# Kernel optimization log

Measured on AMD Instinct MI355X. Metric: run time of the kernel, lower is better.

## Reference

```python
import jax, jax.numpy as jnp
import numpy as np

B, S, D, H = 2, 2048, 1024, 16
HD = D // H  # head dim = 64


def setup_inputs() -> dict:
    key = jax.random.key(0)
    ks = jax.random.split(key, 9)
    sc = 1.0 / np.sqrt(D)
    x = jax.random.normal(ks[0], (B, S, D), dtype=jnp.float32)
    # weights stored as (in, out); y = x @ W + b (same math as torch Linear with W.T)
    Wq = jax.random.normal(ks[1], (D, D), dtype=jnp.float32) * sc
    Wk = jax.random.normal(ks[2], (D, D), dtype=jnp.float32) * sc
    Wv = jax.random.normal(ks[3], (D, D), dtype=jnp.float32) * sc
    Wo = jax.random.normal(ks[4], (D, D), dtype=jnp.float32) * sc
    bq = jax.random.normal(ks[5], (D,), dtype=jnp.float32) * 0.01
    bk = jax.random.normal(ks[6], (D,), dtype=jnp.float32) * 0.01
    bv = jax.random.normal(ks[7], (D,), dtype=jnp.float32) * 0.01
    bo = jax.random.normal(ks[8], (D,), dtype=jnp.float32) * 0.01
    return {"x": x, "Wq": Wq, "bq": bq, "Wk": Wk, "bk": bk,
            "Wv": Wv, "bv": bv, "Wo": Wo, "bo": bo}


def reference(x, Wq, bq, Wk, bk, Wv, bv, Wo, bo):
    b, s, d = x.shape
    q = (x @ Wq + bq).reshape(b, s, H, HD)
    k = (x @ Wk + bk).reshape(b, s, H, HD)
    v = (x @ Wv + bv).reshape(b, s, H, HD)
    # [b, h, s, s] scores, scaled by sqrt(head_dim)
    scores = jnp.einsum('bqhd,bkhd->bhqk', q, k) / np.sqrt(HD)
    causal = jnp.triu(jnp.ones((s, s), dtype=bool), k=1)  # True above diagonal
    scores = jnp.where(causal, -jnp.inf, scores)
    w = jax.nn.softmax(scores, axis=-1)  # dropout rate 0 -> identity
    ctx = jnp.einsum('bhqk,bkhd->bqhd', w, v).reshape(b, s, d)
    return ctx @ Wo + bo
```

## Files before the change

kernel.cpp:

```cpp
#include <hip/hip_runtime.h>
#include <math.h>

#define BB 2
#define SS 2048
#define DD 1024
#define HH 16
#define HDIM 64

typedef __bf16 bf16_t;
typedef __attribute__((ext_vector_type(8))) __bf16 bf16x8;
typedef __attribute__((ext_vector_type(4))) __bf16 bf16x4;
typedef __attribute__((ext_vector_type(4))) float f32x4;

__device__ inline bf16_t f2bf(float f) {
    unsigned int x; __builtin_memcpy(&x, &f, 4);
    unsigned int r = (x + 0x7FFFu + ((x >> 16) & 1u)) >> 16;
    unsigned short us = (unsigned short)r;
    bf16_t b; __builtin_memcpy(&b, &us, 2); return b;
}
__device__ inline unsigned int fbits(float f) {
    unsigned int x; __builtin_memcpy(&x, &f, 4); return x;
}
__device__ inline unsigned int pack_bf2(float a, float b) {
    return ((fbits(a) + 0x8000u) >> 16) | ((fbits(b) + 0x8000u) & 0xFFFF0000u);
}
__device__ inline void gload16(const void* g, void* lds_base) {
    __builtin_amdgcn_global_load_lds(
        (const __attribute__((address_space(1))) void*)g,
        (__attribute__((address_space(3))) void*)lds_base, 16, 0, 0);
}

__global__ __launch_bounds__(256)
void prep_kernel(const float* __restrict__ x, bf16_t* __restrict__ xb,
                 const float* __restrict__ W0, const float* __restrict__ W1,
                 const float* __restrict__ W2, const float* __restrict__ W3,
                 bf16x8* __restrict__ P0, bf16x8* __restrict__ P1,
                 bf16x8* __restrict__ P2, bf16x8* __restrict__ P3) {
    const int bid = blockIdx.x, tid = threadIdx.x;
    if (bid < 2048) {
        const int i = bid * 512 + tid;
        #pragma unroll
        for (int u = 0; u < 2; ++u) {
            const int j = i + u * 256;
            const float4 v = reinterpret_cast<const float4*>(x)[j];
            bf16x4 o;
            o.x = f2bf(v.x); o.y = f2bf(v.y); o.z = f2bf(v.z); o.w = f2bf(v.w);
            reinterpret_cast<bf16x4*>(xb)[j] = o;
        }
    } else {
        const int t = (bid - 2048) * 256 + tid;
        const int g = t >> 10, n = t & 1023;
        const float* Ws[4] = {W0, W1, W2, W3};
        bf16x8* Pp[4] = {P0, P1, P2, P3};
        #pragma unroll
        for (int m = 0; m < 4; ++m) {
            bf16x8 v;
            #pragma unroll
            for (int j = 0; j < 8; ++j) v[j] = f2bf(Ws[m][(size_t)(g * 8 + j) * DD + n]);
            Pp[m][(size_t)g * DD + n] = v;
        }
    }
}

__global__ __launch_bounds__(256)
void gemm_qkv(const bf16_t* __restrict__ A,
              const bf16x8* __restrict__ Wp0, const bf16x8* __restrict__ Wp1,
              const bf16x8* __restrict__ Wp2,
              const float* __restrict__ b0, const float* __restrict__ b1,
              const float* __restrict__ b2,
              bf16_t* __restrict__ C0, bf16_t* __restrict__ C1,
              bf16_t* __restrict__ Vt) {
    __shared__ bf16x8 smem_v[4096];
    char* const smem = (char*)smem_v;

    const int z = blockIdx.z;
    const bf16x8* Wp = (z == 0) ? Wp0 : (z == 1) ? Wp1 : Wp2;
    const float* bias = (z == 0) ? b0 : (z == 1) ? b1 : b2;

    const int tid = threadIdx.x;
    const int ln = tid & 63, wv = tid >> 6;
    const int quad = ln >> 4, l15 = ln & 15;
    const int wr = wv >> 1, wc = wv & 1;
    const int m0 = blockIdx.y * 128;
    const int n0 = blockIdx.x * 128;

    int arow[4], acl[4], bg[4], bn[4];
    #pragma unroll
    for (int u = 0; u < 4; ++u) {
        const int S = (wv * 4 + u) * 64 + ln;
        arow[u] = S >> 3; acl[u] = (S & 7) ^ (arow[u] & 7);
        bg[u] = S >> 7;   bn[u] = S & 127;
    }

    f32x4 acc[4][4];
    #pragma unroll
    for (int i = 0; i < 4; ++i)
        #pragma unroll
        for (int j = 0; j < 4; ++j) acc[i][j] = (f32x4){0.f, 0.f, 0.f, 0.f};

    auto stage = [&](int k0, int buf) {
        char* const base = smem + buf * 32768;
        const int kg0 = k0 >> 3;
        #pragma unroll
        for (int u = 0; u < 4; ++u) {
            gload16(&A[(size_t)(m0 + arow[u]) * DD + k0 + acl[u] * 8],
                    base + (size_t)(wv * 4 + u) * 1024);
            gload16(&Wp[(size_t)(kg0 + bg[u]) * DD + n0 + bn[u]],
                    base + 16384 + (size_t)(wv * 4 + u) * 1024);
        }
    };

    stage(0, 0);
    __syncthreads();
    int cur = 0;
    for (int t = 0; t < 16; ++t) {
        const bf16x8 (*As)[8]   = reinterpret_cast<const bf16x8(*)[8]>(smem + cur * 32768);
        const bf16x8 (*Bs)[128] = reinterpret_cast<const bf16x8(*)[128]>(smem + cur * 32768 + 16384);
        bf16x8 fa[2][4], fb[2][4];
        #pragma unroll
        for (int kk = 0; kk < 2; ++kk) {
            #pragma unroll
            for (int mi = 0; mi < 4; ++mi) {
                const int row = wr * 64 + mi * 16 + l15;
                fa[kk][mi] = As[row][(kk * 4 + quad) ^ (row & 7)];
            }
            #pragma unroll
            for (int ni = 0; ni < 4; ++ni)
                fb[kk][ni] = Bs[kk * 4 + quad][wc * 64 + ni * 16 + l15];
        }
        if (t < 15) stage((t + 1) * 64, cur ^ 1);
        #pragma unroll
        for (int kk = 0; kk < 2; ++kk)
            #pragma unroll
            for (int mi = 0; mi < 4; ++mi)
                #pragma unroll
                for (int ni = 0; ni < 4; ++ni)
                    acc[mi][ni] = __builtin_amdgcn_mfma_f32_16x16x32_bf16(
                        fa[kk][mi], fb[kk][ni], acc[mi][ni], 0, 0, 0);
        if (t < 15) { __syncthreads(); cur ^= 1; }
    }

    if (z < 2) {
        bf16_t* C = (z == 0) ? C0 : C1;
        #pragma unroll
        for (int ni = 0; ni < 4; ++ni) {
            const int col = n0 + wc * 64 + ni * 16 + l15;
            const float bv = bias[col];
            #pragma unroll
            for (int mi = 0; mi < 4; ++mi)
                #pragma unroll
                for (int r = 0; r < 4; ++r) {
                    const int row = m0 + wr * 64 + mi * 16 + quad * 4 + r;
                    C[(size_t)row * DD + col] = f2bf(acc[mi][ni][r] + bv);
                }
        }
    } else {
        unsigned short (*T)[136] = reinterpret_cast<unsigned short(*)[136]>(smem);
        __syncthreads();
        #pragma unroll
        for (int ni = 0; ni < 4; ++ni) {
            const int cl = wc * 64 + ni * 16 + l15;
            const float bv = bias[n0 + cl];
            #pragma unroll
            for (int mi = 0; mi < 4; ++mi) {
                const int rl = wr * 64 + mi * 16 + quad * 4;
                uint2 pk;
                pk.x = pack_bf2(acc[mi][ni][0] + bv, acc[mi][ni][1] + bv);
                pk.y = pack_bf2(acc[mi][ni][2] + bv, acc[mi][ni][3] + bv);
                *reinterpret_cast<uint2*>(&T[cl][rl]) = pk;
            }
        }
        __syncthreads();
        const int b = m0 >> 11, s0 = m0 & 2047, h0 = n0 >> 6;
        #pragma unroll
        for (int u = 0; u < 8; ++u) {
            const int c = u * 256 + tid;
            const int s8 = c & 15, nl = c >> 4;
            const bf16x8 v = *reinterpret_cast<const bf16x8*>(&T[nl][s8 * 8]);
            const int bh = b * 16 + h0 + (nl >> 6), d = nl & 63;
            *reinterpret_cast<bf16x8*>(
                &Vt[((size_t)bh * 64 + d) * SS + s0 + s8 * 8]) = v;
        }
    }
}

__global__ __launch_bounds__(256)
void gemm_out(const bf16_t* __restrict__ A, const bf16x8* __restrict__ Wp,
              const float* __restrict__ bias, float* __restrict__ C) {
    __shared__ bf16x8 As[2][128][8];
    __shared__ bf16x8 Bs[2][8][64];

    const int tid = threadIdx.x;
    const int ln = tid & 63, wv = tid >> 6;
    const int quad = ln >> 4, l15 = ln & 15;
    const int wr = wv >> 1, wc = wv & 1;
    const int m0 = blockIdx.y * 128;
    const int n0 = blockIdx.x * 64;

    int arow[4], acl[4], bkg[2], bn[2];
    #pragma unroll
    for (int u = 0; u < 4; ++u) {
        const int S = (wv * 4 + u) * 64 + ln;
        arow[u] = S >> 3; acl[u] = (S & 7) ^ (arow[u] & 7);
    }
    #pragma unroll
    for (int u = 0; u < 2; ++u) {
        const int S = (wv * 2 + u) * 64 + ln;
        bkg[u] = S >> 6; bn[u] = S & 63;
    }

    f32x4 acc[4][2];
    #pragma unroll
    for (int i = 0; i < 4; ++i)
        #pragma unroll
        for (int j = 0; j < 2; ++j) acc[i][j] = (f32x4){0.f, 0.f, 0.f, 0.f};

    auto stage = [&](int k0, int buf) {
        const int kg0 = k0 >> 3;
        #pragma unroll
        for (int u = 0; u < 4; ++u)
            gload16(&A[(size_t)(m0 + arow[u]) * DD + k0 + acl[u] * 8],
                    (char*)&As[buf][0][0] + (size_t)(wv * 4 + u) * 1024);
        #pragma unroll
        for (int u = 0; u < 2; ++u)
            gload16(&Wp[(size_t)(kg0 + bkg[u]) * DD + n0 + bn[u]],
                    (char*)&Bs[buf][0][0] + (size_t)(wv * 2 + u) * 1024);
    };

    stage(0, 0);
    __syncthreads();
    int cur = 0;
    for (int t = 0; t < 16; ++t) {
        bf16x8 fa[2][4], fb[2][2];
        #pragma unroll
        for (int kk = 0; kk < 2; ++kk) {
            #pragma unroll
            for (int mi = 0; mi < 4; ++mi) {
                const int row = wr * 64 + mi * 16 + l15;
                fa[kk][mi] = As[cur][row][(kk * 4 + quad) ^ (row & 7)];
            }
            #pragma unroll
            for (int ni = 0; ni < 2; ++ni)
                fb[kk][ni] = Bs[cur][kk * 4 + quad][wc * 32 + ni * 16 + l15];
        }
        if (t < 15) stage((t + 1) * 64, cur ^ 1);
        #pragma unroll
        for (int kk = 0; kk < 2; ++kk)
            #pragma unroll
            for (int mi = 0; mi < 4; ++mi)
                #pragma unroll
                for (int ni = 0; ni < 2; ++ni)
                    acc[mi][ni] = __builtin_amdgcn_mfma_f32_16x16x32_bf16(
                        fa[kk][mi], fb[kk][ni], acc[mi][ni], 0, 0, 0);
        if (t < 15) { __syncthreads(); cur ^= 1; }
    }

    #pragma unroll
    for (int ni = 0; ni < 2; ++ni) {
        const int col = n0 + wc * 32 + ni * 16 + l15;
        const float bv = bias[col];
        #pragma unroll
        for (int mi = 0; mi < 4; ++mi)
            #pragma unroll
            for (int r = 0; r < 4; ++r) {
                const int row = m0 + wr * 64 + mi * 16 + quad * 4 + r;
                C[(size_t)row * DD + col] = acc[mi][ni][r] + bv;
            }
    }
}

#define SCL 0.18033688f
#define FM  12.0f

__global__ __launch_bounds__(256)
void attn_mfma(const bf16_t* __restrict__ Q, const bf16_t* __restrict__ Kg,
               const bf16_t* __restrict__ Vt, bf16_t* __restrict__ Ctx) {
    __shared__ bf16x8 Ks[2][128][8];
    __shared__ bf16x8 Vs[2][128][8];
    __shared__ unsigned short Ps[4][2][16][64];

    const int tid = threadIdx.x;
    const int ln = tid & 63, w = tid >> 6;
    const int quad = ln >> 4, l15 = ln & 15;
    const int bh = blockIdx.x;
    const int tswz = (blockIdx.x + blockIdx.y) & 7;
    const int qt = (blockIdx.y < 8) ? tswz : 15 - tswz;
    const int b = bh >> 4, h = bh & 15;
    const size_t rowbase = (size_t)b * SS;
    const int col0 = h * 64;

    const int krow0 = w * 16 + (ln >> 3);
    const int krow1 = krow0 + 8;
    const int kc0 = (ln & 7) ^ (krow0 & 7);
    const int kc1 = (ln & 7) ^ (krow1 & 7);

    bf16x8 fq[2][2];
    #pragma unroll
    for (int rg = 0; rg < 2; ++rg) {
        const int qrow = qt * 128 + w * 32 + rg * 16 + l15;
        #pragma unroll
        for (int kk = 0; kk < 2; ++kk)
            fq[rg][kk] = *reinterpret_cast<const bf16x8*>(
                &Q[(rowbase + qrow) * DD + col0 + kk * 32 + quad * 8]);
    }

    f32x4 acc_o[2][4];
    #pragma unroll
    for (int rg = 0; rg < 2; ++rg)
        #pragma unroll
        for (int i = 0; i < 4; ++i) acc_o[rg][i] = (f32x4){0.f, 0.f, 0.f, 0.f};
    float lsum[2] = {0.f, 0.f};

    auto stage = [&](int tile, int half, int buf) {
        char* kb = (char*)&Ks[buf][half * 64][0] + w * 2048;
        char* vb = (char*)&Vs[buf][half * 64][0] + w * 2048;
        gload16(&Kg[(rowbase + tile * 64 + krow0) * DD + col0 + kc0 * 8], kb);
        gload16(&Kg[(rowbase + tile * 64 + krow1) * DD + col0 + kc1 * 8], kb + 1024);
        gload16(&Vt[((size_t)bh * 64 + krow0) * SS + tile * 64 + kc0 * 8], vb);
        gload16(&Vt[((size_t)bh * 64 + krow1) * SS + tile * 64 + kc1 * 8], vb + 1024);
    };

    const int swz = l15 & 7;

    auto compute_tile = [&](int buf, int ro, int dq0, int dq1) {
        const int dq[2] = {dq0, dq1};
        #pragma unroll
        for (int rg = 0; rg < 2; ++rg) {
            if (dq[rg] < 0) continue;
            unsigned short* const psw = &Ps[w][rg][l15][0];
            #pragma unroll
            for (int ni = 0; ni < 4; ++ni) {
                const int slot = ni * 4 + quad;
                unsigned short* pdst = psw + (((slot >> 1) ^ swz) * 8 + (slot & 1) * 4);
                const int g = ni * 16;
                if (g > dq[rg]) {
                    *reinterpret_cast<uint2*>(pdst) = (uint2){0u, 0u};
                    continue;
                }
                f32x4 st = (f32x4){0.f, 0.f, 0.f, 0.f};
                const int krow = ni * 16 + l15;
                #pragma unroll
                for (int kk = 0; kk < 2; ++kk) {
                    const bf16x8 fk = Ks[buf][ro + krow][(kk * 4 + quad) ^ (krow & 7)];
                    st = __builtin_amdgcn_mfma_f32_16x16x32_bf16(fk, fq[rg][kk], st, 0, 0, 0);
                }
                float p[4];
                #pragma unroll
                for (int r = 0; r < 4; ++r) {
                    p[r] = __builtin_amdgcn_exp2f(st[r] * SCL - FM);
                    if (g == dq[rg] && (quad * 4 + r) > l15) p[r] = 0.f;
                }
                lsum[rg] += (p[0] + p[1]) + (p[2] + p[3]);
                uint2 pk;
                pk.x = pack_bf2(p[0], p[1]);
                pk.y = pack_bf2(p[2], p[3]);
                *reinterpret_cast<uint2*>(pdst) = pk;
            }
        }
        #pragma unroll
        for (int kk = 0; kk < 2; ++kk) {
            bf16x8 fp[2];
            #pragma unroll
            for (int rg = 0; rg < 2; ++rg)
                fp[rg] = *reinterpret_cast<const bf16x8*>(
                    &Ps[w][rg][l15][(((kk * 4 + quad) ^ swz) * 8)]);
            #pragma unroll
            for (int nd = 0; nd < 4; ++nd) {
                const int vrow = nd * 16 + l15;
                const bf16x8 fv = Vs[buf][ro + vrow][(kk * 4 + quad) ^ (vrow & 7)];
                if (dq0 >= 0)
                    acc_o[0][nd] = __builtin_amdgcn_mfma_f32_16x16x32_bf16(fv, fp[0], acc_o[0][nd], 0, 0, 0);
                if (dq1 >= 0)
                    acc_o[1][nd] = __builtin_amdgcn_mfma_f32_16x16x32_bf16(fv, fp[1], acc_o[1][nd], 0, 0, 0);
            }
        }
    };

    stage(0, 0, 0);
    stage(1, 1, 0);
    __syncthreads();
    int cur = 0;
    for (int p = 0; p < qt; ++p) {
        stage(2 * (p + 1), 0, cur ^ 1);
        stage(2 * (p + 1) + 1, 1, cur ^ 1);
        compute_tile(cur, 0, 112, 112);
        compute_tile(cur, 64, 112, 112);
        __syncthreads();
        cur ^= 1;
    }
    {
        const int lq0 = w * 32, lq1 = w * 32 + 16;
        compute_tile(cur, 0, lq0, lq1);
        compute_tile(cur, 64, lq0 - 64, lq1 - 64);
    }

    #pragma unroll
    for (int rg = 0; rg < 2; ++rg) {
        float s = lsum[rg];
        s += __shfl_xor(s, 16);
        s += __shfl_xor(s, 32);
        const float inv = 1.f / s;
        const size_t orow = (rowbase + qt * 128 + w * 32 + rg * 16 + l15) * DD + col0;
        #pragma unroll
        for (int nd = 0; nd < 4; ++nd) {
            uint2 ov;
            ov.x = pack_bf2(acc_o[rg][nd][0] * inv, acc_o[rg][nd][1] * inv);
            ov.y = pack_bf2(acc_o[rg][nd][2] * inv, acc_o[rg][nd][3] * inv);
            *reinterpret_cast<uint2*>(&Ctx[orow + nd * 16 + quad * 4]) = ov;
        }
    }
}

extern "C" void kernel_launch(void* const* d_in, const int* in_sizes, int n_in,
                              void* d_out, int out_size, void* d_ws, size_t ws_size,
                              hipStream_t stream) {
    const float* x  = (const float*)d_in[0];
    const float* Wq = (const float*)d_in[1];
    const float* bq = (const float*)d_in[2];
    const float* Wk = (const float*)d_in[3];
    const float* bk = (const float*)d_in[4];
    const float* Wv = (const float*)d_in[5];
    const float* bv = (const float*)d_in[6];
    const float* Wo = (const float*)d_in[7];
    const float* bo = (const float*)d_in[8];
    float* out = (float*)d_out;

    const size_t M = (size_t)BB * SS;
    const size_t mat = M * DD;
    const size_t wsz = (size_t)DD * DD;

    bf16_t* ws = (bf16_t*)d_ws;
    bf16_t* xb   = ws;
    bf16_t* Wqp  = ws + mat;
    bf16_t* Wkp  = Wqp + wsz;
    bf16_t* Wvp  = Wkp + wsz;
    bf16_t* Wop  = Wvp + wsz;
    bf16_t* Qb   = Wop + wsz;
    bf16_t* Kb   = Qb + mat;
    bf16_t* Vtb  = Kb + mat;
    bf16_t* Ctxb = Vtb + mat;

    dim3 blk(256);
    hipLaunchKernelGGL(prep_kernel, dim3(2560), blk, 0, stream,
                       x, xb, Wq, Wk, Wv, Wo,
                       (bf16x8*)Wqp, (bf16x8*)Wkp, (bf16x8*)Wvp, (bf16x8*)Wop);

    hipLaunchKernelGGL(gemm_qkv, dim3(DD / 128, M / 128, 3), blk, 0, stream,
                       xb, (const bf16x8*)Wqp, (const bf16x8*)Wkp, (const bf16x8*)Wvp,
                       bq, bk, bv, Qb, Kb, Vtb);

    hipLaunchKernelGGL(attn_mfma, dim3(BB * HH, SS / 128), blk, 0, stream,
                       Qb, Kb, Vtb, Ctxb);

    hipLaunchKernelGGL(gemm_out, dim3(DD / 64, M / 128), blk, 0, stream,
                       Ctxb, (const bf16x8*)Wop, bo, out);
}
```

Measured before the change: 188.8 us.

## Remap grids for XCD-aware locality and halve attention query tile to 64

```diff
diff --git a/kernel.cpp b/kernel.cpp
--- a/kernel.cpp
+++ b/kernel.cpp
@@ -73,7 +73,13 @@
     __shared__ bf16x8 smem_v[4096];
     char* const smem = (char*)smem_v;
 
-    const int z = blockIdx.z;
+    const int f = blockIdx.x;
+    const int xcd = f & 7, l = f >> 3;
+    const int ytile = xcd * 4 + (l & 3);
+    const int zx = l >> 2;
+    const int z = zx >> 3;
+    const int xtile = zx & 7;
+
     const bf16x8* Wp = (z == 0) ? Wp0 : (z == 1) ? Wp1 : Wp2;
     const float* bias = (z == 0) ? b0 : (z == 1) ? b1 : b2;
 
@@ -81,8 +87,8 @@
     const int ln = tid & 63, wv = tid >> 6;
     const int quad = ln >> 4, l15 = ln & 15;
     const int wr = wv >> 1, wc = wv & 1;
-    const int m0 = blockIdx.y * 128;
-    const int n0 = blockIdx.x * 128;
+    const int m0 = ytile * 128;
+    const int n0 = xtile * 128;
 
     int arow[4], acl[4], bg[4], bn[4];
     #pragma unroll
@@ -190,12 +196,17 @@
     __shared__ bf16x8 As[2][128][8];
     __shared__ bf16x8 Bs[2][8][64];
 
+    const int f = blockIdx.x;
+    const int xcd = f & 7, l = f >> 3;
+    const int ytile = xcd * 4 + (l & 3);
+    const int xtile = l >> 2;
+
     const int tid = threadIdx.x;
     const int ln = tid & 63, wv = tid >> 6;
     const int quad = ln >> 4, l15 = ln & 15;
     const int wr = wv >> 1, wc = wv & 1;
-    const int m0 = blockIdx.y * 128;
-    const int n0 = blockIdx.x * 64;
+    const int m0 = ytile * 128;
+    const int n0 = xtile * 64;
 
     int arow[4], acl[4], bkg[2], bn[2];
     #pragma unroll
@@ -275,16 +286,21 @@
 __global__ __launch_bounds__(256)
 void attn_mfma(const bf16_t* __restrict__ Q, const bf16_t* __restrict__ Kg,
                const bf16_t* __restrict__ Vt, bf16_t* __restrict__ Ctx) {
-    __shared__ bf16x8 Ks[2][128][8];
-    __shared__ bf16x8 Vs[2][128][8];
-    __shared__ unsigned short Ps[4][2][16][64];
+    __shared__ bf16x8 Ks[2][64][8];
+    __shared__ bf16x8 Vs[2][64][8];
+    __shared__ unsigned short Ps[4][16][64];
 
     const int tid = threadIdx.x;
     const int ln = tid & 63, w = tid >> 6;
     const int quad = ln >> 4, l15 = ln & 15;
-    const int bh = blockIdx.x;
-    const int tswz = (blockIdx.x + blockIdx.y) & 7;
-    const int qt = (blockIdx.y < 8) ? tswz : 15 - tswz;
+
+    const int f = blockIdx.x;
+    const int xcd = f & 7, l = f >> 3;
+    const int bh = xcd * 4 + (l & 3);
+    const int ytile = l >> 2;
+    const int tswz = (bh + ytile) & 15;
+    const int qt = (ytile < 16) ? tswz : 31 - tswz;
+
     const int b = bh >> 4, h = bh & 15;
     const size_t rowbase = (size_t)b * SS;
     const int col0 = h * 64;
@@ -294,26 +310,21 @@
     const int kc0 = (ln & 7) ^ (krow0 & 7);
     const int kc1 = (ln & 7) ^ (krow1 & 7);
 
-    bf16x8 fq[2][2];
-    #pragma unroll
-    for (int rg = 0; rg < 2; ++rg) {
-        const int qrow = qt * 128 + w * 32 + rg * 16 + l15;
-        #pragma unroll
-        for (int kk = 0; kk < 2; ++kk)
-            fq[rg][kk] = *reinterpret_cast<const bf16x8*>(
-                &Q[(rowbase + qrow) * DD + col0 + kk * 32 + quad * 8]);
-    }
-
-    f32x4 acc_o[2][4];
-    #pragma unroll
-    for (int rg = 0; rg < 2; ++rg)
-        #pragma unroll
-        for (int i = 0; i < 4; ++i) acc_o[rg][i] = (f32x4){0.f, 0.f, 0.f, 0.f};
-    float lsum[2] = {0.f, 0.f};
-
-    auto stage = [&](int tile, int half, int buf) {
-        char* kb = (char*)&Ks[buf][half * 64][0] + w * 2048;
-        char* vb = (char*)&Vs[buf][half * 64][0] + w * 2048;
+    bf16x8 fq[2];
+    const int qrow = qt * 64 + w * 16 + l15;
+    #pragma unroll
+    for (int kk = 0; kk < 2; ++kk)
+        fq[kk] = *reinterpret_cast<const bf16x8*>(
+            &Q[(rowbase + qrow) * DD + col0 + kk * 32 + quad * 8]);
+
+    f32x4 acc_o[4];
+    #pragma unroll
+    for (int i = 0; i < 4; ++i) acc_o[i] = (f32x4){0.f, 0.f, 0.f, 0.f};
+    float lsum = 0.f;
+
+    auto stage = [&](int tile, int buf) {
+        char* kb = (char*)&Ks[buf][0][0] + w * 2048;
+        char* vb = (char*)&Vs[buf][0][0] + w * 2048;
         gload16(&Kg[(rowbase + tile * 64 + krow0) * DD + col0 + kc0 * 8], kb);
         gload16(&Kg[(rowbase + tile * 64 + krow1) * DD + col0 + kc1 * 8], kb + 1024);
         gload16(&Vt[((size_t)bh * 64 + krow0) * SS + tile * 64 + kc0 * 8], vb);
@@ -322,90 +333,71 @@
 
     const int swz = l15 & 7;
 
-    auto compute_tile = [&](int buf, int ro, int dq0, int dq1) {
-        const int dq[2] = {dq0, dq1};
-        #pragma unroll
-        for (int rg = 0; rg < 2; ++rg) {
-            if (dq[rg] < 0) continue;
-            unsigned short* const psw = &Ps[w][rg][l15][0];
-            #pragma unroll
-            for (int ni = 0; ni < 4; ++ni) {
-                const int slot = ni * 4 + quad;
-                unsigned short* pdst = psw + (((slot >> 1) ^ swz) * 8 + (slot & 1) * 4);
-                const int g = ni * 16;
-                if (g > dq[rg]) {
-                    *reinterpret_cast<uint2*>(pdst) = (uint2){0u, 0u};
-                    continue;
-                }
-                f32x4 st = (f32x4){0.f, 0.f, 0.f, 0.f};
-                const int krow = ni * 16 + l15;
-                #pragma unroll
-                for (int kk = 0; kk < 2; ++kk) {
-                    const bf16x8 fk = Ks[buf][ro + krow][(kk * 4 + quad) ^ (krow & 7)];
-                    st = __builtin_amdgcn_mfma_f32_16x16x32_bf16(fk, fq[rg][kk], st, 0, 0, 0);
-                }
-                float p[4];
-                #pragma unroll
-                for (int r = 0; r < 4; ++r) {
-                    p[r] = __builtin_amdgcn_exp2f(st[r] * SCL - FM);
-                    if (g == dq[rg] && (quad * 4 + r) > l15) p[r] = 0.f;
-                }
-                lsum[rg] += (p[0] + p[1]) + (p[2] + p[3]);
-                uint2 pk;
-                pk.x = pack_bf2(p[0], p[1]);
-                pk.y = pack_bf2(p[2], p[3]);
-                *reinterpret_cast<uint2*>(pdst) = pk;
-            }
+    auto compute_tile = [&](int buf, int dq) {
+        unsigned short* const psw = &Ps[w][l15][0];
+        #pragma unroll
+        for (int ni = 0; ni < 4; ++ni) {
+            const int slot = ni * 4 + quad;
+            unsigned short* pdst = psw + (((slot >> 1) ^ swz) * 8 + (slot & 1) * 4);
+            const int g = ni * 16;
+            if (g > dq) {
+                *reinterpret_cast<uint2*>(pdst) = (uint2){0u, 0u};
+                continue;
+            }
+            f32x4 st = (f32x4){0.f, 0.f, 0.f, 0.f};
+            const int krow = ni * 16 + l15;
+            #pragma unroll
+            for (int kk = 0; kk < 2; ++kk) {
+                const bf16x8 fk = Ks[buf][krow][(kk * 4 + quad) ^ (krow & 7)];
+                st = __builtin_amdgcn_mfma_f32_16x16x32_bf16(fk, fq[kk], st, 0, 0, 0);
+            }
+            float p[4];
+            #pragma unroll
+            for (int r = 0; r < 4; ++r) {
+                p[r] = __builtin_amdgcn_exp2f(st[r] * SCL - FM);
+                if (g == dq && (quad * 4 + r) > l15) p[r] = 0.f;
+            }
+            lsum += (p[0] + p[1]) + (p[2] + p[3]);
+            uint2 pk;
+            pk.x = pack_bf2(p[0], p[1]);
+            pk.y = pack_bf2(p[2], p[3]);
+            *reinterpret_cast<uint2*>(pdst) = pk;
         }
         #pragma unroll
         for (int kk = 0; kk < 2; ++kk) {
-            bf16x8 fp[2];
-            #pragma unroll
-            for (int rg = 0; rg < 2; ++rg)
-                fp[rg] = *reinterpret_cast<const bf16x8*>(
-                    &Ps[w][rg][l15][(((kk * 4 + quad) ^ swz) * 8)]);
+            const bf16x8 fp = *reinterpret_cast<const bf16x8*>(
+                &Ps[w][l15][(((kk * 4 + quad) ^ swz) * 8)]);
             #pragma unroll
             for (int nd = 0; nd < 4; ++nd) {
                 const int vrow = nd * 16 + l15;
-                const bf16x8 fv = Vs[buf][ro + vrow][(kk * 4 + quad) ^ (vrow & 7)];
-                if (dq0 >= 0)
-                    acc_o[0][nd] = __builtin_amdgcn_mfma_f32_16x16x32_bf16(fv, fp[0], acc_o[0][nd], 0, 0, 0);
-                if (dq1 >= 0)
-                    acc_o[1][nd] = __builtin_amdgcn_mfma_f32_16x16x32_bf16(fv, fp[1], acc_o[1][nd], 0, 0, 0);
+                const bf16x8 fv = Vs[buf][vrow][(kk * 4 + quad) ^ (vrow & 7)];
+                acc_o[nd] = __builtin_amdgcn_mfma_f32_16x16x32_bf16(fv, fp, acc_o[nd], 0, 0, 0);
             }
         }
     };
 
-    stage(0, 0, 0);
-    stage(1, 1, 0);
+    stage(0, 0);
     __syncthreads();
     int cur = 0;
-    for (int p = 0; p < qt; ++p) {
-        stage(2 * (p + 1), 0, cur ^ 1);
-        stage(2 * (p + 1) + 1, 1, cur ^ 1);
-        compute_tile(cur, 0, 112, 112);
-        compute_tile(cur, 64, 112, 112);
+    for (int t = 0; t < qt; ++t) {
+        stage(t + 1, cur ^ 1);
+        compute_tile(cur, 112);
         __syncthreads();
         cur ^= 1;
     }
+    compute_tile(cur, w * 16);
+
     {
-        const int lq0 = w * 32, lq1 = w * 32 + 16;
-        compute_tile(cur, 0, lq0, lq1);
-        compute_tile(cur, 64, lq0 - 64, lq1 - 64);
-    }
-
-    #pragma unroll
-    for (int rg = 0; rg < 2; ++rg) {
-        float s = lsum[rg];
+        float s = lsum;
         s += __shfl_xor(s, 16);
         s += __shfl_xor(s, 32);
         const float inv = 1.f / s;
-        const size_t orow = (rowbase + qt * 128 + w * 32 + rg * 16 + l15) * DD + col0;
+        const size_t orow = (rowbase + qrow) * DD + col0;
         #pragma unroll
         for (int nd = 0; nd < 4; ++nd) {
             uint2 ov;
-            ov.x = pack_bf2(acc_o[rg][nd][0] * inv, acc_o[rg][nd][1] * inv);
-            ov.y = pack_bf2(acc_o[rg][nd][2] * inv, acc_o[rg][nd][3] * inv);
+            ov.x = pack_bf2(acc_o[nd][0] * inv, acc_o[nd][1] * inv);
+            ov.y = pack_bf2(acc_o[nd][2] * inv, acc_o[nd][3] * inv);
             *reinterpret_cast<uint2*>(&Ctx[orow + nd * 16 + quad * 4]) = ov;
         }
     }
@@ -445,13 +437,13 @@
                        x, xb, Wq, Wk, Wv, Wo,
                        (bf16x8*)Wqp, (bf16x8*)Wkp, (bf16x8*)Wvp, (bf16x8*)Wop);
 
-    hipLaunchKernelGGL(gemm_qkv, dim3(DD / 128, M / 128, 3), blk, 0, stream,
+    hipLaunchKernelGGL(gemm_qkv, dim3(768), blk, 0, stream,
                        xb, (const bf16x8*)Wqp, (const bf16x8*)Wkp, (const bf16x8*)Wvp,
                        bq, bk, bv, Qb, Kb, Vtb);
 
-    hipLaunchKernelGGL(attn_mfma, dim3(BB * HH, SS / 128), blk, 0, stream,
+    hipLaunchKernelGGL(attn_mfma, dim3(1024), blk, 0, stream,
                        Qb, Kb, Vtb, Ctxb);
 
-    hipLaunchKernelGGL(gemm_out, dim3(DD / 64, M / 128), blk, 0, stream,
+    hipLaunchKernelGGL(gemm_out, dim3(512), blk, 0, stream,
                        Ctxb, (const bf16x8*)Wop, bo, out);
 }
```

After: 188.3 us. Within noise of the previous version (-0.2%).
